# Performance work log

Measured on AMD Instinct MI355X. Metric: run time of the kernel, lower is better.

Reference implementation:

```python
import jax, jax.numpy as jnp
import numpy as np
import math

B, S, D, H, P = 4, 2048, 512, 8, 64
HD = D // H


def setup_inputs() -> dict:
    key = jax.random.key(0)
    ks = jax.random.split(key, 12)
    inp = {
        "query": jax.random.normal(ks[0], (B, S, D), jnp.float32),
        "key": jax.random.normal(ks[1], (B, S, D), jnp.float32),
        "value": jax.random.normal(ks[2], (B, S, D), jnp.float32),
        "query_pos_em": jax.random.normal(ks[3], (B, S, P), jnp.float32),
        "key_pos_em": jax.random.normal(ks[4], (B, S, P), jnp.float32),
        "mask": jax.random.randint(ks[5], (B, S), 0, 2, jnp.int32),
        # learned params (bias=False linears, LayerNorm affine)
        "Wq": jax.random.normal(ks[6], (D, D), jnp.float32) / math.sqrt(D),
        "Wk": jax.random.normal(ks[7], (D, D), jnp.float32) / math.sqrt(D),
        "Wv": jax.random.normal(ks[8], (D, D), jnp.float32) / math.sqrt(D),
        "Wo": jax.random.normal(ks[9], (D, D), jnp.float32) / math.sqrt(D),
        "ln_gamma": jnp.ones((D,), jnp.float32),
        "ln_beta": jnp.zeros((D,), jnp.float32),
    }
    return inp


def _split_heads(x):
    # (B,S,D) -> (B,H,S,HD)
    return x.reshape(B, S, H, HD).transpose(0, 2, 1, 3)


def reference(query, key, value, query_pos_em, key_pos_em, mask,
              Wq, Wk, Wv, Wo, ln_gamma, ln_beta):
    residual = query
    q = _split_heads(query @ Wq)
    k = _split_heads(key @ Wk)
    v = _split_heads(value @ Wv)

    # positional similarity: softmax over (B,S,S)
    simi = jax.nn.softmax(jnp.einsum('bqp,bkp->bqk', query_pos_em, key_pos_em), axis=-1)

    # scaled dot-product modulated elementwise by similarity (broadcast over heads)
    prod = jnp.einsum('bhqd,bhkd->bhqk', q, k) / math.sqrt(HD)
    prod = prod * simi[:, None, :, :]

    # additive mask: (mask-1)*1e8, broadcast [:, None, None, :]
    m = (mask.astype(prod.dtype) - 1.0) * 1e8
    prod = prod + m[:, None, None, :]

    attn = jax.nn.softmax(prod, axis=-1)
    out = jnp.einsum('bhqk,bhkd->bhqd', attn, v)  # (B,H,S,HD)
    out = out.transpose(0, 2, 1, 3).reshape(B, S, D)
    out = out @ Wo  # dropout is identity in eval mode

    x = residual + out
    mu = jnp.mean(x, axis=-1, keepdims=True)
    var = jnp.var(x, axis=-1, keepdims=True)
    return (x - mu) / jnp.sqrt(var + 1e-5) * ln_gamma + ln_beta
```

## Files before the change

kernel.cpp:

```cpp
#include <hip/hip_runtime.h>
#include <hip/hip_bf16.h>

#define Bq 4
#define Sq 2048
#define Dq 512
#define Hq 8
#define HDq 64
#define Pq 64

typedef __attribute__((ext_vector_type(8))) short short8;
typedef __attribute__((ext_vector_type(4))) float f32x4;

__device__ inline unsigned short f2bf(float f) {
  unsigned int u = __float_as_uint(f);
  unsigned int r = u + 0x7FFFu + ((u >> 16) & 1u);
  return (unsigned short)(r >> 16);
}
__device__ inline float bf2f(unsigned short s) {
  return __uint_as_float(((unsigned int)s) << 16);
}
__device__ inline short8 ld8f(const float* __restrict__ p) {
  const float4 a = *(const float4*)p;
  const float4 b = *(const float4*)(p + 4);
  short8 r;
  r[0] = (short)f2bf(a.x); r[1] = (short)f2bf(a.y); r[2] = (short)f2bf(a.z); r[3] = (short)f2bf(a.w);
  r[4] = (short)f2bf(b.x); r[5] = (short)f2bf(b.y); r[6] = (short)f2bf(b.z); r[7] = (short)f2bf(b.w);
  return r;
}

__global__ __launch_bounds__(256) void prep(const float* __restrict__ qpe,
                                            const float* __restrict__ kpe,
                                            const int* __restrict__ mask,
                                            unsigned short* __restrict__ qpeb,
                                            unsigned short* __restrict__ kpeb,
                                            float* __restrict__ mb) {
  const int bid = blockIdx.x;
  if (bid < 256) {
    int i = bid * 256 + threadIdx.x;
    *(short8*)&qpeb[(size_t)i * 8] = ld8f(qpe + (size_t)i * 8);
  } else if (bid < 512) {
    int i = (bid - 256) * 256 + threadIdx.x;
    *(short8*)&kpeb[(size_t)i * 8] = ld8f(kpe + (size_t)i * 8);
  } else {
    int i = (bid - 512) * 256 + threadIdx.x;
    mb[i] = ((float)mask[i] - 1.0f) * 1.442695041e8f;
  }
}

__global__ __launch_bounds__(256) void convW4(const float* __restrict__ Wq,
                                              const float* __restrict__ Wk,
                                              const float* __restrict__ Wv,
                                              const float* __restrict__ Wo,
                                              unsigned short* __restrict__ Wqt,
                                              unsigned short* __restrict__ Wkt,
                                              unsigned short* __restrict__ Wvt,
                                              unsigned short* __restrict__ Wot) {
  __shared__ float tile[32][33];
  const int z = blockIdx.z;
  const float* W = z == 0 ? Wq : z == 1 ? Wk : z == 2 ? Wv : Wo;
  unsigned short* Wt = z == 0 ? Wqt : z == 1 ? Wkt : z == 2 ? Wvt : Wot;
  const float scale = (z == 0) ? 0.125f : 1.0f;
  const int tx = threadIdx.x & 31, ty = threadIdx.x >> 5;
  const int n0 = blockIdx.x * 32, k0 = blockIdx.y * 32;
  for (int j = 0; j < 4; ++j)
    tile[ty + j * 8][tx] = W[(size_t)(k0 + ty + j * 8) * Dq + n0 + tx];
  __syncthreads();
  for (int j = 0; j < 4; ++j)
    Wt[(size_t)(n0 + ty + j * 8) * Dq + k0 + tx] = f2bf(tile[tx][ty + j * 8] * scale);
}

__global__ __launch_bounds__(256) void gemm_qkv(const float* __restrict__ Aq,
                                                const float* __restrict__ Ak,
                                                const float* __restrict__ Av,
                                                const unsigned short* __restrict__ Wqt,
                                                const unsigned short* __restrict__ Wkt,
                                                const unsigned short* __restrict__ Wvt,
                                                unsigned short* __restrict__ Qb,
                                                unsigned short* __restrict__ Kb,
                                                unsigned short* __restrict__ VbT) {
  __shared__ unsigned short Alds[128][72];
  __shared__ unsigned short Blds[128][72];
  const int z = blockIdx.z;
  const float* Ap = z == 0 ? Aq : z == 1 ? Ak : Av;
  const unsigned short* Wt = z == 0 ? Wqt : z == 1 ? Wkt : Wvt;
  unsigned short* Cb = z == 0 ? Qb : z == 1 ? Kb : VbT;
  const bool wt = (z == 2);
  const int tid = threadIdx.x;
  const int lane = tid & 63, wv = tid >> 6;
  const int wr = wv >> 1, wc = wv & 1;
  const int l15 = lane & 15, lg = lane >> 4;
  const int row0 = blockIdx.x * 128, col0 = blockIdx.y * 128;
  f32x4 acc[4][4] = {};
  for (int k0 = 0; k0 < Dq; k0 += 64) {
    __syncthreads();
#pragma unroll
    for (int j = 0; j < 4; ++j) {
      int s = tid + j * 256;
      int r = s >> 3, c8 = (s & 7) * 8;
      const float* ap = Ap + (size_t)(row0 + r) * Dq + k0 + c8;
      float4 f0 = *(const float4*)ap;
      float4 f1 = *(const float4*)(ap + 4);
      short8 u;
      u[0] = (short)f2bf(f0.x); u[1] = (short)f2bf(f0.y);
      u[2] = (short)f2bf(f0.z); u[3] = (short)f2bf(f0.w);
      u[4] = (short)f2bf(f1.x); u[5] = (short)f2bf(f1.y);
      u[6] = (short)f2bf(f1.z); u[7] = (short)f2bf(f1.w);
      *(short8*)&Alds[r][c8] = u;
      *(uint4*)&Blds[r][c8] = *(const uint4*)&Wt[(size_t)(col0 + r) * Dq + k0 + c8];
    }
    __syncthreads();
#pragma unroll
    for (int kc = 0; kc < 2; ++kc) {
      short8 a[4], b[4];
#pragma unroll
      for (int mi = 0; mi < 4; ++mi)
        a[mi] = *(const short8*)&Alds[wr * 64 + mi * 16 + l15][kc * 32 + lg * 8];
#pragma unroll
      for (int ni = 0; ni < 4; ++ni)
        b[ni] = *(const short8*)&Blds[wc * 64 + ni * 16 + l15][kc * 32 + lg * 8];
#pragma unroll
      for (int mi = 0; mi < 4; ++mi)
#pragma unroll
        for (int ni = 0; ni < 4; ++ni)
          acc[mi][ni] = __builtin_amdgcn_mfma_f32_16x16x32_bf16(a[mi], b[ni], acc[mi][ni], 0, 0, 0);
    }
  }
  const int orow = row0 + wr * 64 + lg * 4;
  const int ocol = col0 + wc * 64 + l15;
  if (wt) {
    const int bidx = orow >> 11;
#pragma unroll
    for (int mi = 0; mi < 4; ++mi)
#pragma unroll
      for (int ni = 0; ni < 4; ++ni) {
        int gc = ocol + ni * 16;
        int s = (orow + mi * 16) & (Sq - 1);
        ushort4 w = {f2bf(acc[mi][ni][0]), f2bf(acc[mi][ni][1]),
                     f2bf(acc[mi][ni][2]), f2bf(acc[mi][ni][3])};
        *(ushort4*)&Cb[((size_t)(bidx * Dq + gc)) * Sq + s] = w;
      }
  } else {
#pragma unroll
    for (int mi = 0; mi < 4; ++mi)
#pragma unroll
      for (int ni = 0; ni < 4; ++ni)
#pragma unroll
        for (int rr = 0; rr < 4; ++rr) {
          int gr = orow + mi * 16 + rr, gc = ocol + ni * 16;
          Cb[(size_t)gr * Dq + gc] = f2bf(acc[mi][ni][rr]);
        }
  }
}

__global__ __launch_bounds__(256) void gemm_wo(const unsigned short* __restrict__ Ab,
                                               const unsigned short* __restrict__ Wt,
                                               const float* __restrict__ res,
                                               float* __restrict__ Cf) {
  __shared__ unsigned short Alds[128][72];
  __shared__ unsigned short Blds[128][72];
  const int tid = threadIdx.x;
  const int lane = tid & 63, wv = tid >> 6;
  const int wr = wv >> 1, wc = wv & 1;
  const int l15 = lane & 15, lg = lane >> 4;
  const int row0 = blockIdx.x * 128, col0 = blockIdx.y * 128;
  f32x4 acc[4][4] = {};
  for (int k0 = 0; k0 < Dq; k0 += 64) {
    __syncthreads();
#pragma unroll
    for (int j = 0; j < 4; ++j) {
      int s = tid + j * 256;
      int r = s >> 3, c8 = (s & 7) * 8;
      *(uint4*)&Alds[r][c8] = *(const uint4*)&Ab[(size_t)(row0 + r) * Dq + k0 + c8];
      *(uint4*)&Blds[r][c8] = *(const uint4*)&Wt[(size_t)(col0 + r) * Dq + k0 + c8];
    }
    __syncthreads();
#pragma unroll
    for (int kc = 0; kc < 2; ++kc) {
      short8 a[4], b[4];
#pragma unroll
      for (int mi = 0; mi < 4; ++mi)
        a[mi] = *(const short8*)&Alds[wr * 64 + mi * 16 + l15][kc * 32 + lg * 8];
#pragma unroll
      for (int ni = 0; ni < 4; ++ni)
        b[ni] = *(const short8*)&Blds[wc * 64 + ni * 16 + l15][kc * 32 + lg * 8];
#pragma unroll
      for (int mi = 0; mi < 4; ++mi)
#pragma unroll
        for (int ni = 0; ni < 4; ++ni)
          acc[mi][ni] = __builtin_amdgcn_mfma_f32_16x16x32_bf16(a[mi], b[ni], acc[mi][ni], 0, 0, 0);
    }
  }
  const int orow = row0 + wr * 64 + lg * 4;
  const int ocol = col0 + wc * 64 + l15;
#pragma unroll
  for (int mi = 0; mi < 4; ++mi)
#pragma unroll
    for (int ni = 0; ni < 4; ++ni)
#pragma unroll
      for (int rr = 0; rr < 4; ++rr) {
        int gr = orow + mi * 16 + rr, gc = ocol + ni * 16;
        Cf[(size_t)gr * Dq + gc] = acc[mi][ni][rr] + res[(size_t)gr * Dq + gc];
      }
}

__global__ __launch_bounds__(256) void possim(const unsigned short* __restrict__ qpe,
                                              const unsigned short* __restrict__ kpe,
                                              unsigned short* __restrict__ simiB,
                                              float* __restrict__ invsum) {
  __shared__ float wsum[4][16];
  const int tid = threadIdx.x, lane = tid & 63, wv = tid >> 6;
  const int l15 = lane & 15, lg = lane >> 4;
  const int b = blockIdx.y, q0 = blockIdx.x * 16;
  const unsigned short* qrow = qpe + ((size_t)(b * Sq + q0 + l15)) * Pq + lg * 8;
  short8 aq0 = *(const short8*)qrow;
  short8 aq1 = *(const short8*)(qrow + 32);
  unsigned short* sB = simiB + ((size_t)(b * (Sq / 16) + blockIdx.x)) * Sq * 16;
  float lsum[4] = {0.f, 0.f, 0.f, 0.f};
  for (int t = wv; t < Sq / 64; t += 4) {
    int k0 = t * 64;
    f32x4 sc[4] = {};
#pragma unroll
    for (int ng = 0; ng < 4; ++ng) {
      const unsigned short* krow = kpe + ((size_t)(b * Sq + k0 + ng * 16 + l15)) * Pq + lg * 8;
      short8 bk0 = *(const short8*)krow;
      short8 bk1 = *(const short8*)(krow + 32);
      sc[ng] = __builtin_amdgcn_mfma_f32_16x16x32_bf16(aq0, bk0, sc[ng], 0, 0, 0);
      sc[ng] = __builtin_amdgcn_mfma_f32_16x16x32_bf16(aq1, bk1, sc[ng], 0, 0, 0);
    }
#pragma unroll
    for (int ng = 0; ng < 4; ++ng) {
      float e0 = __expf(sc[ng][0]);
      float e1 = __expf(sc[ng][1]);
      float e2 = __expf(sc[ng][2]);
      float e3 = __expf(sc[ng][3]);
      lsum[0] += e0; lsum[1] += e1; lsum[2] += e2; lsum[3] += e3;
      ushort4 st = {f2bf(e0), f2bf(e1), f2bf(e2), f2bf(e3)};
      *(ushort4*)&sB[(size_t)(k0 + ng * 16 + l15) * 16 + lg * 4] = st;
    }
  }
  for (int rr = 0; rr < 4; ++rr)
    for (int m = 1; m < 16; m <<= 1) lsum[rr] += __shfl_xor(lsum[rr], m, 64);
  if (l15 == 0)
    for (int rr = 0; rr < 4; ++rr) wsum[wv][lg * 4 + rr] = lsum[rr];
  __syncthreads();
  if (tid < 16) {
    float tot = wsum[0][tid] + wsum[1][tid] + wsum[2][tid] + wsum[3][tid];
    invsum[b * Sq + q0 + tid] = 1.0f / tot;
  }
}

__global__ __launch_bounds__(512) void attn(const unsigned short* __restrict__ Qb,
                                            const unsigned short* __restrict__ Kb,
                                            const unsigned short* __restrict__ VbT,
                                            const unsigned short* __restrict__ simiB,
                                            const float* __restrict__ invsum,
                                            const float* __restrict__ mbias,
                                            unsigned short* __restrict__ O) {
  __shared__ unsigned short Klds[2][64][72];
  __shared__ unsigned short Vlds[2][64][72];
  __shared__ unsigned short Plds[8][16][72];
  const int tid = threadIdx.x, lane = tid & 63, wv = tid >> 6;
  const int l15 = lane & 15, lg = lane >> 4;
  const int q0 = blockIdx.x * 128, h = blockIdx.y, b = blockIdx.z;
  const int qw = q0 + wv * 16;
  const int sr = tid >> 3, sc8 = (tid & 7) * 8;
  const unsigned short* Kg = Kb + ((size_t)(b * Sq + sr)) * Dq + h * HDq + sc8;
  const unsigned short* Vg = VbT + ((size_t)(b * Dq + h * HDq + sr)) * Sq + sc8;

  const unsigned short* qp = Qb + ((size_t)(b * Sq + qw + l15)) * Dq + h * HDq + lg * 8;
  short8 aq0 = *(const short8*)qp;
  short8 aq1 = *(const short8*)(qp + 32);
  float inv2[4];
#pragma unroll
  for (int rr = 0; rr < 4; ++rr)
    inv2[rr] = invsum[b * Sq + qw + lg * 4 + rr] * 1.442695041f;
  const unsigned short* sB =
      simiB + ((size_t)(b * (Sq / 16) + blockIdx.x * 8 + wv)) * Sq * 16 + lg * 4;
  const float* Mb = mbias + b * Sq;
  const int wxor = (lg >> 1) << 3;
  const int lgs = lg ^ (l15 >> 3);

  {
    *(uint4*)&Klds[0][sr][sc8] = *(const uint4*)Kg;
    *(uint4*)&Vlds[0][sr][sc8] = *(const uint4*)Vg;
  }
  f32x4 oacc[4] = {};
  float lsum[4] = {0.f, 0.f, 0.f, 0.f};
  int cur = 0;
  for (int t = 0; t < Sq / 64; ++t) {
    const int k0 = t * 64;
    __syncthreads();
    uint4 nk0, nv0;
    const bool more = (t < Sq / 64 - 1);
    if (more) {
      nk0 = *(const uint4*)(Kg + (size_t)(k0 + 64) * Dq);
      nv0 = *(const uint4*)(Vg + (k0 + 64));
    }
    ushort4 sv4[4];
    float mbf[4];
#pragma unroll
    for (int ng = 0; ng < 4; ++ng) {
      int kk = k0 + ng * 16 + l15;
      sv4[ng] = *(const ushort4*)&sB[(size_t)kk * 16];
      mbf[ng] = Mb[kk];
    }
    f32x4 sc[4] = {};
    __builtin_amdgcn_s_setprio(1);
#pragma unroll
    for (int ng = 0; ng < 4; ++ng) {
      short8 bk0 = *(const short8*)&Klds[cur][ng * 16 + l15][lg * 8];
      short8 bk1 = *(const short8*)&Klds[cur][ng * 16 + l15][32 + lg * 8];
      sc[ng] = __builtin_amdgcn_mfma_f32_16x16x32_bf16(aq0, bk0, sc[ng], 0, 0, 0);
      sc[ng] = __builtin_amdgcn_mfma_f32_16x16x32_bf16(aq1, bk1, sc[ng], 0, 0, 0);
    }
    __builtin_amdgcn_s_setprio(0);
#pragma unroll
    for (int ng = 0; ng < 4; ++ng) {
#pragma unroll
      for (int rr = 0; rr < 4; ++rr) {
        float sv = bf2f(rr == 0 ? sv4[ng].x : rr == 1 ? sv4[ng].y : rr == 2 ? sv4[ng].z
                                                                            : sv4[ng].w);
        float p = __builtin_amdgcn_exp2f(fmaf(sc[ng][rr] * sv, inv2[rr], mbf[ng]));
        lsum[rr] += p;
        Plds[wv][lg * 4 + rr][ng * 16 + (l15 ^ wxor)] = f2bf(p);
      }
    }
    short8 pa0 = *(const short8*)&Plds[wv][l15][lgs * 8];
    short8 pa1 = *(const short8*)&Plds[wv][l15][32 + lgs * 8];
    __builtin_amdgcn_s_setprio(1);
#pragma unroll
    for (int dg = 0; dg < 4; ++dg) {
      short8 bv0 = *(const short8*)&Vlds[cur][dg * 16 + l15][lg * 8];
      short8 bv1 = *(const short8*)&Vlds[cur][dg * 16 + l15][32 + lg * 8];
      oacc[dg] = __builtin_amdgcn_mfma_f32_16x16x32_bf16(pa0, bv0, oacc[dg], 0, 0, 0);
      oacc[dg] = __builtin_amdgcn_mfma_f32_16x16x32_bf16(pa1, bv1, oacc[dg], 0, 0, 0);
    }
    __builtin_amdgcn_s_setprio(0);
    if (more) {
      *(uint4*)&Klds[cur ^ 1][sr][sc8] = nk0;
      *(uint4*)&Vlds[cur ^ 1][sr][sc8] = nv0;
      cur ^= 1;
    }
  }
#pragma unroll
  for (int rr = 0; rr < 4; ++rr)
    for (int m = 1; m < 16; m <<= 1) lsum[rr] += __shfl_xor(lsum[rr], m, 64);
#pragma unroll
  for (int dg = 0; dg < 4; ++dg)
    for (int rr = 0; rr < 4; ++rr) {
      int qg = qw + lg * 4 + rr;
      O[((size_t)(b * Sq + qg)) * Dq + h * HDq + dg * 16 + l15] = f2bf(oacc[dg][rr] / lsum[rr]);
    }
}

__global__ __launch_bounds__(256) void lnorm(float* __restrict__ X,
                                             const float* __restrict__ gamma,
                                             const float* __restrict__ beta) {
  const int tid = threadIdx.x, lane = tid & 63, wv = tid >> 6;
  const int row = blockIdx.x * 4 + wv;
  float* xr = X + (size_t)row * Dq + lane * 8;
  float4 x0 = *(float4*)xr;
  float4 x1 = *(float4*)(xr + 4);
  float s = x0.x + x0.y + x0.z + x0.w + x1.x + x1.y + x1.z + x1.w;
  float s2 = x0.x * x0.x + x0.y * x0.y + x0.z * x0.z + x0.w * x0.w +
             x1.x * x1.x + x1.y * x1.y + x1.z * x1.z + x1.w * x1.w;
  for (int m = 1; m < 64; m <<= 1) {
    s += __shfl_xor(s, m, 64);
    s2 += __shfl_xor(s2, m, 64);
  }
  float mu = s * (1.0f / 512.0f);
  float var = s2 * (1.0f / 512.0f) - mu * mu;
  float rstd = rsqrtf(var + 1e-5f);
  const float* g = gamma + lane * 8;
  const float* be = beta + lane * 8;
  float4 y0, y1;
  y0.x = (x0.x - mu) * rstd * g[0] + be[0];
  y0.y = (x0.y - mu) * rstd * g[1] + be[1];
  y0.z = (x0.z - mu) * rstd * g[2] + be[2];
  y0.w = (x0.w - mu) * rstd * g[3] + be[3];
  y1.x = (x1.x - mu) * rstd * g[4] + be[4];
  y1.y = (x1.y - mu) * rstd * g[5] + be[5];
  y1.z = (x1.z - mu) * rstd * g[6] + be[6];
  y1.w = (x1.w - mu) * rstd * g[7] + be[7];
  *(float4*)xr = y0;
  *(float4*)(xr + 4) = y1;
}

extern "C" void kernel_launch(void* const* d_in, const int* in_sizes, int n_in,
                              void* d_out, int out_size, void* d_ws, size_t ws_size,
                              hipStream_t stream) {
  const float* query = (const float*)d_in[0];
  const float* key = (const float*)d_in[1];
  const float* value = (const float*)d_in[2];
  const float* qpe = (const float*)d_in[3];
  const float* kpe = (const float*)d_in[4];
  const int* mask = (const int*)d_in[5];
  const float* Wq = (const float*)d_in[6];
  const float* Wk = (const float*)d_in[7];
  const float* Wv = (const float*)d_in[8];
  const float* Wo = (const float*)d_in[9];
  const float* gamma = (const float*)d_in[10];
  const float* beta = (const float*)d_in[11];
  float* out = (float*)d_out;

  char* ws = (char*)d_ws;
  size_t off = 0;
  unsigned short* Qb = (unsigned short*)(ws + off); off += (size_t)Bq * Sq * Dq * 2;
  unsigned short* Kb = (unsigned short*)(ws + off); off += (size_t)Bq * Sq * Dq * 2;
  unsigned short* VbT = (unsigned short*)(ws + off); off += (size_t)Bq * Sq * Dq * 2;
  unsigned short* Wqt = (unsigned short*)(ws + off); off += (size_t)Dq * Dq * 2;
  unsigned short* Wkt = (unsigned short*)(ws + off); off += (size_t)Dq * Dq * 2;
  unsigned short* Wvt = (unsigned short*)(ws + off); off += (size_t)Dq * Dq * 2;
  unsigned short* Wot = (unsigned short*)(ws + off); off += (size_t)Dq * Dq * 2;
  unsigned short* simiB = (unsigned short*)(ws + off); off += (size_t)Bq * Sq * Sq * 2;
  float* invsum = (float*)(ws + off); off += (size_t)Bq * Sq * 4;
  float* mbias = (float*)(ws + off); off += (size_t)Bq * Sq * 4;
  unsigned short* Ob = (unsigned short*)(ws + off); off += (size_t)Bq * Sq * Dq * 2;
  unsigned short* qpeb = (unsigned short*)(ws + off); off += (size_t)Bq * Sq * Pq * 2;
  unsigned short* kpeb = (unsigned short*)(ws + off); off += (size_t)Bq * Sq * Pq * 2;

  dim3 blk(256);
  prep<<<dim3(544), blk, 0, stream>>>(qpe, kpe, mask, qpeb, kpeb, mbias);
  convW4<<<dim3(16, 16, 4), blk, 0, stream>>>(Wq, Wk, Wv, Wo, Wqt, Wkt, Wvt, Wot);
  possim<<<dim3(Sq / 16, Bq), blk, 0, stream>>>(qpeb, kpeb, simiB, invsum);
  gemm_qkv<<<dim3(64, 4, 3), blk, 0, stream>>>(query, key, value, Wqt, Wkt, Wvt, Qb, Kb, VbT);
  attn<<<dim3(Sq / 128, Hq, Bq), dim3(512), 0, stream>>>(Qb, Kb, VbT, simiB, invsum, mbias, Ob);
  gemm_wo<<<dim3(64, 4), blk, 0, stream>>>(Ob, Wot, query, out);
  lnorm<<<dim3(Bq * Sq / 4), blk, 0, stream>>>(out, gamma, beta);
}
```

Baseline: 149.1 us.

## Merge independent prep and GEMM launches, register-prefetch GEMM tiles and attention inputs

Folds the prep and weight-conversion kernels into one launch, and the positional-similarity and QKV GEMM kernels into another heterogeneous launch, cutting launches from seven to five so independent work can share the GPU. The QKV and Wo GEMMs now prefetch the next K-slab from global memory into registers while the current slab is computed. The attention kernel prefetches the next tile's similarity and mask values one iteration ahead. It also drops the XOR swizzle on the P tile in LDS, which may bring back LDS bank conflicts, and the extra prefetch registers raise register pressure.

```diff
diff --git a/kernel.cpp b/kernel.cpp
--- a/kernel.cpp
+++ b/kernel.cpp
@@ -28,12 +28,21 @@
   return r;
 }
 
-__global__ __launch_bounds__(256) void prep(const float* __restrict__ qpe,
-                                            const float* __restrict__ kpe,
-                                            const int* __restrict__ mask,
-                                            unsigned short* __restrict__ qpeb,
-                                            unsigned short* __restrict__ kpeb,
-                                            float* __restrict__ mb) {
+__global__ __launch_bounds__(256) void prep_conv(const float* __restrict__ qpe,
+                                                 const float* __restrict__ kpe,
+                                                 const int* __restrict__ mask,
+                                                 const float* __restrict__ Wq,
+                                                 const float* __restrict__ Wk,
+                                                 const float* __restrict__ Wv,
+                                                 const float* __restrict__ Wo,
+                                                 unsigned short* __restrict__ qpeb,
+                                                 unsigned short* __restrict__ kpeb,
+                                                 float* __restrict__ mb,
+                                                 unsigned short* __restrict__ Wqt,
+                                                 unsigned short* __restrict__ Wkt,
+                                                 unsigned short* __restrict__ Wvt,
+                                                 unsigned short* __restrict__ Wot) {
+  __shared__ float tile[32][33];
   const int bid = blockIdx.x;
   if (bid < 256) {
     int i = bid * 256 + threadIdx.x;
@@ -41,114 +50,173 @@
   } else if (bid < 512) {
     int i = (bid - 256) * 256 + threadIdx.x;
     *(short8*)&kpeb[(size_t)i * 8] = ld8f(kpe + (size_t)i * 8);
-  } else {
+  } else if (bid < 544) {
     int i = (bid - 512) * 256 + threadIdx.x;
     mb[i] = ((float)mask[i] - 1.0f) * 1.442695041e8f;
-  }
-}
-
-__global__ __launch_bounds__(256) void convW4(const float* __restrict__ Wq,
-                                              const float* __restrict__ Wk,
-                                              const float* __restrict__ Wv,
-                                              const float* __restrict__ Wo,
-                                              unsigned short* __restrict__ Wqt,
-                                              unsigned short* __restrict__ Wkt,
-                                              unsigned short* __restrict__ Wvt,
-                                              unsigned short* __restrict__ Wot) {
-  __shared__ float tile[32][33];
-  const int z = blockIdx.z;
-  const float* W = z == 0 ? Wq : z == 1 ? Wk : z == 2 ? Wv : Wo;
-  unsigned short* Wt = z == 0 ? Wqt : z == 1 ? Wkt : z == 2 ? Wvt : Wot;
-  const float scale = (z == 0) ? 0.125f : 1.0f;
-  const int tx = threadIdx.x & 31, ty = threadIdx.x >> 5;
-  const int n0 = blockIdx.x * 32, k0 = blockIdx.y * 32;
-  for (int j = 0; j < 4; ++j)
-    tile[ty + j * 8][tx] = W[(size_t)(k0 + ty + j * 8) * Dq + n0 + tx];
-  __syncthreads();
-  for (int j = 0; j < 4; ++j)
-    Wt[(size_t)(n0 + ty + j * 8) * Dq + k0 + tx] = f2bf(tile[tx][ty + j * 8] * scale);
-}
-
-__global__ __launch_bounds__(256) void gemm_qkv(const float* __restrict__ Aq,
-                                                const float* __restrict__ Ak,
-                                                const float* __restrict__ Av,
-                                                const unsigned short* __restrict__ Wqt,
-                                                const unsigned short* __restrict__ Wkt,
-                                                const unsigned short* __restrict__ Wvt,
-                                                unsigned short* __restrict__ Qb,
-                                                unsigned short* __restrict__ Kb,
-                                                unsigned short* __restrict__ VbT) {
+  } else {
+    const int cid = bid - 544;
+    const int x = cid & 15, y = (cid >> 4) & 15, z = cid >> 8;
+    const float* W = z == 0 ? Wq : z == 1 ? Wk : z == 2 ? Wv : Wo;
+    unsigned short* Wt = z == 0 ? Wqt : z == 1 ? Wkt : z == 2 ? Wvt : Wot;
+    const float scale = (z == 0) ? 0.125f : 1.0f;
+    const int tx = threadIdx.x & 31, ty = threadIdx.x >> 5;
+    const int n0 = x * 32, k0 = y * 32;
+    for (int j = 0; j < 4; ++j)
+      tile[ty + j * 8][tx] = W[(size_t)(k0 + ty + j * 8) * Dq + n0 + tx];
+    __syncthreads();
+    for (int j = 0; j < 4; ++j)
+      Wt[(size_t)(n0 + ty + j * 8) * Dq + k0 + tx] = f2bf(tile[tx][ty + j * 8] * scale);
+  }
+}
+
+__global__ __launch_bounds__(256) void sim_qkv(const float* __restrict__ Aq,
+                                               const float* __restrict__ Ak,
+                                               const float* __restrict__ Av,
+                                               const unsigned short* __restrict__ Wqt,
+                                               const unsigned short* __restrict__ Wkt,
+                                               const unsigned short* __restrict__ Wvt,
+                                               unsigned short* __restrict__ Qb,
+                                               unsigned short* __restrict__ Kb,
+                                               unsigned short* __restrict__ VbT,
+                                               const unsigned short* __restrict__ qpe,
+                                               const unsigned short* __restrict__ kpe,
+                                               unsigned short* __restrict__ simiB,
+                                               float* __restrict__ invsum) {
   __shared__ unsigned short Alds[128][72];
   __shared__ unsigned short Blds[128][72];
-  const int z = blockIdx.z;
-  const float* Ap = z == 0 ? Aq : z == 1 ? Ak : Av;
-  const unsigned short* Wt = z == 0 ? Wqt : z == 1 ? Wkt : Wvt;
-  unsigned short* Cb = z == 0 ? Qb : z == 1 ? Kb : VbT;
-  const bool wt = (z == 2);
+  __shared__ float wsum[4][16];
+  const int bid = blockIdx.x;
   const int tid = threadIdx.x;
   const int lane = tid & 63, wv = tid >> 6;
-  const int wr = wv >> 1, wc = wv & 1;
   const int l15 = lane & 15, lg = lane >> 4;
-  const int row0 = blockIdx.x * 128, col0 = blockIdx.y * 128;
-  f32x4 acc[4][4] = {};
-  for (int k0 = 0; k0 < Dq; k0 += 64) {
-    __syncthreads();
+  if (bid < 768) {
+    const int z = bid >> 8, rem = bid & 255;
+    const int bx = rem & 63, by = rem >> 6;
+    const float* Ap = z == 0 ? Aq : z == 1 ? Ak : Av;
+    const unsigned short* Wt = z == 0 ? Wqt : z == 1 ? Wkt : Wvt;
+    unsigned short* Cb = z == 0 ? Qb : z == 1 ? Kb : VbT;
+    const bool wt = (z == 2);
+    const int wr = wv >> 1, wc = wv & 1;
+    const int row0 = bx * 128, col0 = by * 128;
+    f32x4 acc[4][4] = {};
+    float4 fA0[4], fA1[4];
+    uint4 fB[4];
 #pragma unroll
     for (int j = 0; j < 4; ++j) {
       int s = tid + j * 256;
       int r = s >> 3, c8 = (s & 7) * 8;
-      const float* ap = Ap + (size_t)(row0 + r) * Dq + k0 + c8;
-      float4 f0 = *(const float4*)ap;
-      float4 f1 = *(const float4*)(ap + 4);
-      short8 u;
-      u[0] = (short)f2bf(f0.x); u[1] = (short)f2bf(f0.y);
-      u[2] = (short)f2bf(f0.z); u[3] = (short)f2bf(f0.w);
-      u[4] = (short)f2bf(f1.x); u[5] = (short)f2bf(f1.y);
-      u[6] = (short)f2bf(f1.z); u[7] = (short)f2bf(f1.w);
-      *(short8*)&Alds[r][c8] = u;
-      *(uint4*)&Blds[r][c8] = *(const uint4*)&Wt[(size_t)(col0 + r) * Dq + k0 + c8];
-    }
+      const float* ap = Ap + (size_t)(row0 + r) * Dq + c8;
+      fA0[j] = *(const float4*)ap;
+      fA1[j] = *(const float4*)(ap + 4);
+      fB[j] = *(const uint4*)&Wt[(size_t)(col0 + r) * Dq + c8];
+    }
+    for (int k0 = 0; k0 < Dq; k0 += 64) {
+      __syncthreads();
+#pragma unroll
+      for (int j = 0; j < 4; ++j) {
+        int s = tid + j * 256;
+        int r = s >> 3, c8 = (s & 7) * 8;
+        short8 u;
+        u[0] = (short)f2bf(fA0[j].x); u[1] = (short)f2bf(fA0[j].y);
+        u[2] = (short)f2bf(fA0[j].z); u[3] = (short)f2bf(fA0[j].w);
+        u[4] = (short)f2bf(fA1[j].x); u[5] = (short)f2bf(fA1[j].y);
+        u[6] = (short)f2bf(fA1[j].z); u[7] = (short)f2bf(fA1[j].w);
+        *(short8*)&Alds[r][c8] = u;
+        *(uint4*)&Blds[r][c8] = fB[j];
+      }
+      __syncthreads();
+      if (k0 + 64 < Dq) {
+#pragma unroll
+        for (int j = 0; j < 4; ++j) {
+          int s = tid + j * 256;
+          int r = s >> 3, c8 = (s & 7) * 8;
+          const float* ap = Ap + (size_t)(row0 + r) * Dq + k0 + 64 + c8;
+          fA0[j] = *(const float4*)ap;
+          fA1[j] = *(const float4*)(ap + 4);
+          fB[j] = *(const uint4*)&Wt[(size_t)(col0 + r) * Dq + k0 + 64 + c8];
+        }
+      }
+#pragma unroll
+      for (int kc = 0; kc < 2; ++kc) {
+        short8 a[4], b[4];
+#pragma unroll
+        for (int mi = 0; mi < 4; ++mi)
+          a[mi] = *(const short8*)&Alds[wr * 64 + mi * 16 + l15][kc * 32 + lg * 8];
+#pragma unroll
+        for (int ni = 0; ni < 4; ++ni)
+          b[ni] = *(const short8*)&Blds[wc * 64 + ni * 16 + l15][kc * 32 + lg * 8];
+#pragma unroll
+        for (int mi = 0; mi < 4; ++mi)
+#pragma unroll
+          for (int ni = 0; ni < 4; ++ni)
+            acc[mi][ni] = __builtin_amdgcn_mfma_f32_16x16x32_bf16(a[mi], b[ni], acc[mi][ni], 0, 0, 0);
+      }
+    }
+    const int orow = row0 + wr * 64 + lg * 4;
+    const int ocol = col0 + wc * 64 + l15;
+    if (wt) {
+      const int bidx = orow >> 11;
+#pragma unroll
+      for (int mi = 0; mi < 4; ++mi)
+#pragma unroll
+        for (int ni = 0; ni < 4; ++ni) {
+          int gc = ocol + ni * 16;
+          int s = (orow + mi * 16) & (Sq - 1);
+          ushort4 w = {f2bf(acc[mi][ni][0]), f2bf(acc[mi][ni][1]),
+                       f2bf(acc[mi][ni][2]), f2bf(acc[mi][ni][3])};
+          *(ushort4*)&Cb[((size_t)(bidx * Dq + gc)) * Sq + s] = w;
+        }
+    } else {
+#pragma unroll
+      for (int mi = 0; mi < 4; ++mi)
+#pragma unroll
+        for (int ni = 0; ni < 4; ++ni)
+#pragma unroll
+          for (int rr = 0; rr < 4; ++rr) {
+            int gr = orow + mi * 16 + rr, gc = ocol + ni * 16;
+            Cb[(size_t)gr * Dq + gc] = f2bf(acc[mi][ni][rr]);
+          }
+    }
+  } else {
+    const int pbid = bid - 768;
+    const int qblk = pbid & 127, b = pbid >> 7;
+    const int q0 = qblk * 16;
+    const unsigned short* qrow = qpe + ((size_t)(b * Sq + q0 + l15)) * Pq + lg * 8;
+    short8 aq0 = *(const short8*)qrow;
+    short8 aq1 = *(const short8*)(qrow + 32);
+    unsigned short* sB = simiB + ((size_t)(b * (Sq / 16) + qblk)) * Sq * 16;
+    float lsum[4] = {0.f, 0.f, 0.f, 0.f};
+    for (int t = wv; t < Sq / 64; t += 4) {
+      int k0 = t * 64;
+      f32x4 sc[4] = {};
+#pragma unroll
+      for (int ng = 0; ng < 4; ++ng) {
+        const unsigned short* krow = kpe + ((size_t)(b * Sq + k0 + ng * 16 + l15)) * Pq + lg * 8;
+        short8 bk0 = *(const short8*)krow;
+        short8 bk1 = *(const short8*)(krow + 32);
+        sc[ng] = __builtin_amdgcn_mfma_f32_16x16x32_bf16(aq0, bk0, sc[ng], 0, 0, 0);
+        sc[ng] = __builtin_amdgcn_mfma_f32_16x16x32_bf16(aq1, bk1, sc[ng], 0, 0, 0);
+      }
+#pragma unroll
+      for (int ng = 0; ng < 4; ++ng) {
+        float e0 = __expf(sc[ng][0]);
+        float e1 = __expf(sc[ng][1]);
+        float e2 = __expf(sc[ng][2]);
+        float e3 = __expf(sc[ng][3]);
+        lsum[0] += e0; lsum[1] += e1; lsum[2] += e2; lsum[3] += e3;
+        ushort4 st = {f2bf(e0), f2bf(e1), f2bf(e2), f2bf(e3)};
+        *(ushort4*)&sB[(size_t)(k0 + ng * 16 + l15) * 16 + lg * 4] = st;
+      }
+    }
+    for (int rr = 0; rr < 4; ++rr)
+      for (int m = 1; m < 16; m <<= 1) lsum[rr] += __shfl_xor(lsum[rr], m, 64);
+    if (l15 == 0)
+      for (int rr = 0; rr < 4; ++rr) wsum[wv][lg * 4 + rr] = lsum[rr];
     __syncthreads();
-#pragma unroll
-    for (int kc = 0; kc < 2; ++kc) {
-      short8 a[4], b[4];
-#pragma unroll
-      for (int mi = 0; mi < 4; ++mi)
-        a[mi] = *(const short8*)&Alds[wr * 64 + mi * 16 + l15][kc * 32 + lg * 8];
-#pragma unroll
-      for (int ni = 0; ni < 4; ++ni)
-        b[ni] = *(const short8*)&Blds[wc * 64 + ni * 16 + l15][kc * 32 + lg * 8];
-#pragma unroll
-      for (int mi = 0; mi < 4; ++mi)
-#pragma unroll
-        for (int ni = 0; ni < 4; ++ni)
-          acc[mi][ni] = __builtin_amdgcn_mfma_f32_16x16x32_bf16(a[mi], b[ni], acc[mi][ni], 0, 0, 0);
-    }
-  }
-  const int orow = row0 + wr * 64 + lg * 4;
-  const int ocol = col0 + wc * 64 + l15;
-  if (wt) {
-    const int bidx = orow >> 11;
-#pragma unroll
-    for (int mi = 0; mi < 4; ++mi)
-#pragma unroll
-      for (int ni = 0; ni < 4; ++ni) {
-        int gc = ocol + ni * 16;
-        int s = (orow + mi * 16) & (Sq - 1);
-        ushort4 w = {f2bf(acc[mi][ni][0]), f2bf(acc[mi][ni][1]),
-                     f2bf(acc[mi][ni][2]), f2bf(acc[mi][ni][3])};
-        *(ushort4*)&Cb[((size_t)(bidx * Dq + gc)) * Sq + s] = w;
-      }
-  } else {
-#pragma unroll
-    for (int mi = 0; mi < 4; ++mi)
-#pragma unroll
-      for (int ni = 0; ni < 4; ++ni)
-#pragma unroll
-        for (int rr = 0; rr < 4; ++rr) {
-          int gr = orow + mi * 16 + rr, gc = ocol + ni * 16;
-          Cb[(size_t)gr * Dq + gc] = f2bf(acc[mi][ni][rr]);
-        }
+    if (tid < 16) {
+      float tot = wsum[0][tid] + wsum[1][tid] + wsum[2][tid] + wsum[3][tid];
+      invsum[b * Sq + q0 + tid] = 1.0f / tot;
+    }
   }
 }
 
@@ -164,16 +232,33 @@
   const int l15 = lane & 15, lg = lane >> 4;
   const int row0 = blockIdx.x * 128, col0 = blockIdx.y * 128;
   f32x4 acc[4][4] = {};
+  uint4 fA[4], fB[4];
+#pragma unroll
+  for (int j = 0; j < 4; ++j) {
+    int s = tid + j * 256;
+    int r = s >> 3, c8 = (s & 7) * 8;
+    fA[j] = *(const uint4*)&Ab[(size_t)(row0 + r) * Dq + c8];
+    fB[j] = *(const uint4*)&Wt[(size_t)(col0 + r) * Dq + c8];
+  }
   for (int k0 = 0; k0 < Dq; k0 += 64) {
     __syncthreads();
 #pragma unroll
     for (int j = 0; j < 4; ++j) {
       int s = tid + j * 256;
       int r = s >> 3, c8 = (s & 7) * 8;
-      *(uint4*)&Alds[r][c8] = *(const uint4*)&Ab[(size_t)(row0 + r) * Dq + k0 + c8];
-      *(uint4*)&Blds[r][c8] = *(const uint4*)&Wt[(size_t)(col0 + r) * Dq + k0 + c8];
+      *(uint4*)&Alds[r][c8] = fA[j];
+      *(uint4*)&Blds[r][c8] = fB[j];
     }
     __syncthreads();
+    if (k0 + 64 < Dq) {
+#pragma unroll
+      for (int j = 0; j < 4; ++j) {
+        int s = tid + j * 256;
+        int r = s >> 3, c8 = (s & 7) * 8;
+        fA[j] = *(const uint4*)&Ab[(size_t)(row0 + r) * Dq + k0 + 64 + c8];
+        fB[j] = *(const uint4*)&Wt[(size_t)(col0 + r) * Dq + k0 + 64 + c8];
+      }
+    }
 #pragma unroll
     for (int kc = 0; kc < 2; ++kc) {
       short8 a[4], b[4];
@@ -201,52 +286,6 @@
         int gr = orow + mi * 16 + rr, gc = ocol + ni * 16;
         Cf[(size_t)gr * Dq + gc] = acc[mi][ni][rr] + res[(size_t)gr * Dq + gc];
       }
-}
-
-__global__ __launch_bounds__(256) void possim(const unsigned short* __restrict__ qpe,
-                                              const unsigned short* __restrict__ kpe,
-                                              unsigned short* __restrict__ simiB,
-                                              float* __restrict__ invsum) {
-  __shared__ float wsum[4][16];
-  const int tid = threadIdx.x, lane = tid & 63, wv = tid >> 6;
-  const int l15 = lane & 15, lg = lane >> 4;
-  const int b = blockIdx.y, q0 = blockIdx.x * 16;
-  const unsigned short* qrow = qpe + ((size_t)(b * Sq + q0 + l15)) * Pq + lg * 8;
-  short8 aq0 = *(const short8*)qrow;
-  short8 aq1 = *(const short8*)(qrow + 32);
-  unsigned short* sB = simiB + ((size_t)(b * (Sq / 16) + blockIdx.x)) * Sq * 16;
-  float lsum[4] = {0.f, 0.f, 0.f, 0.f};
-  for (int t = wv; t < Sq / 64; t += 4) {
-    int k0 = t * 64;
-    f32x4 sc[4] = {};
-#pragma unroll
-    for (int ng = 0; ng < 4; ++ng) {
-      const unsigned short* krow = kpe + ((size_t)(b * Sq + k0 + ng * 16 + l15)) * Pq + lg * 8;
-      short8 bk0 = *(const short8*)krow;
-      short8 bk1 = *(const short8*)(krow + 32);
-      sc[ng] = __builtin_amdgcn_mfma_f32_16x16x32_bf16(aq0, bk0, sc[ng], 0, 0, 0);
-      sc[ng] = __builtin_amdgcn_mfma_f32_16x16x32_bf16(aq1, bk1, sc[ng], 0, 0, 0);
-    }
-#pragma unroll
-    for (int ng = 0; ng < 4; ++ng) {
-      float e0 = __expf(sc[ng][0]);
-      float e1 = __expf(sc[ng][1]);
-      float e2 = __expf(sc[ng][2]);
-      float e3 = __expf(sc[ng][3]);
-      lsum[0] += e0; lsum[1] += e1; lsum[2] += e2; lsum[3] += e3;
-      ushort4 st = {f2bf(e0), f2bf(e1), f2bf(e2), f2bf(e3)};
-      *(ushort4*)&sB[(size_t)(k0 + ng * 16 + l15) * 16 + lg * 4] = st;
-    }
-  }
-  for (int rr = 0; rr < 4; ++rr)
-    for (int m = 1; m < 16; m <<= 1) lsum[rr] += __shfl_xor(lsum[rr], m, 64);
-  if (l15 == 0)
-    for (int rr = 0; rr < 4; ++rr) wsum[wv][lg * 4 + rr] = lsum[rr];
-  __syncthreads();
-  if (tid < 16) {
-    float tot = wsum[0][tid] + wsum[1][tid] + wsum[2][tid] + wsum[3][tid];
-    invsum[b * Sq + q0 + tid] = 1.0f / tot;
-  }
 }
 
 __global__ __launch_bounds__(512) void attn(const unsigned short* __restrict__ Qb,
@@ -277,9 +316,15 @@
   const unsigned short* sB =
       simiB + ((size_t)(b * (Sq / 16) + blockIdx.x * 8 + wv)) * Sq * 16 + lg * 4;
   const float* Mb = mbias + b * Sq;
-  const int wxor = (lg >> 1) << 3;
-  const int lgs = lg ^ (l15 >> 3);
-
+
+  ushort4 sv4[4];
+  float mbf[4];
+#pragma unroll
+  for (int ng = 0; ng < 4; ++ng) {
+    int kk = ng * 16 + l15;
+    sv4[ng] = *(const ushort4*)&sB[(size_t)kk * 16];
+    mbf[ng] = Mb[kk];
+  }
   {
     *(uint4*)&Klds[0][sr][sc8] = *(const uint4*)Kg;
     *(uint4*)&Vlds[0][sr][sc8] = *(const uint4*)Vg;
@@ -291,18 +336,18 @@
     const int k0 = t * 64;
     __syncthreads();
     uint4 nk0, nv0;
+    ushort4 nsv[4];
+    float nmb[4];
     const bool more = (t < Sq / 64 - 1);
     if (more) {
       nk0 = *(const uint4*)(Kg + (size_t)(k0 + 64) * Dq);
       nv0 = *(const uint4*)(Vg + (k0 + 64));
-    }
-    ushort4 sv4[4];
-    float mbf[4];
-#pragma unroll
-    for (int ng = 0; ng < 4; ++ng) {
-      int kk = k0 + ng * 16 + l15;
-      sv4[ng] = *(const ushort4*)&sB[(size_t)kk * 16];
-      mbf[ng] = Mb[kk];
+#pragma unroll
+      for (int ng = 0; ng < 4; ++ng) {
+        int kk = k0 + 64 + ng * 16 + l15;
+        nsv[ng] = *(const ushort4*)&sB[(size_t)kk * 16];
+        nmb[ng] = Mb[kk];
+      }
     }
     f32x4 sc[4] = {};
     __builtin_amdgcn_s_setprio(1);
@@ -322,11 +367,11 @@
                                                                             : sv4[ng].w);
         float p = __builtin_amdgcn_exp2f(fmaf(sc[ng][rr] * sv, inv2[rr], mbf[ng]));
         lsum[rr] += p;
-        Plds[wv][lg * 4 + rr][ng * 16 + (l15 ^ wxor)] = f2bf(p);
-      }
-    }
-    short8 pa0 = *(const short8*)&Plds[wv][l15][lgs * 8];
-    short8 pa1 = *(const short8*)&Plds[wv][l15][32 + lgs * 8];
+        Plds[wv][lg * 4 + rr][ng * 16 + l15] = f2bf(p);
+      }
+    }
+    short8 pa0 = *(const short8*)&Plds[wv][l15][lg * 8];
+    short8 pa1 = *(const short8*)&Plds[wv][l15][32 + lg * 8];
     __builtin_amdgcn_s_setprio(1);
 #pragma unroll
     for (int dg = 0; dg < 4; ++dg) {
@@ -339,6 +384,11 @@
     if (more) {
       *(uint4*)&Klds[cur ^ 1][sr][sc8] = nk0;
       *(uint4*)&Vlds[cur ^ 1][sr][sc8] = nv0;
+#pragma unroll
+      for (int ng = 0; ng < 4; ++ng) {
+        sv4[ng] = nsv[ng];
+        mbf[ng] = nmb[ng];
+      }
       cur ^= 1;
     }
   }
@@ -420,10 +470,10 @@
   unsigned short* kpeb = (unsigned short*)(ws + off); off += (size_t)Bq * Sq * Pq * 2;
 
   dim3 blk(256);
-  prep<<<dim3(544), blk, 0, stream>>>(qpe, kpe, mask, qpeb, kpeb, mbias);
-  convW4<<<dim3(16, 16, 4), blk, 0, stream>>>(Wq, Wk, Wv, Wo, Wqt, Wkt, Wvt, Wot);
-  possim<<<dim3(Sq / 16, Bq), blk, 0, stream>>>(qpeb, kpeb, simiB, invsum);
-  gemm_qkv<<<dim3(64, 4, 3), blk, 0, stream>>>(query, key, value, Wqt, Wkt, Wvt, Qb, Kb, VbT);
+  prep_conv<<<dim3(544 + 1024), blk, 0, stream>>>(qpe, kpe, mask, Wq, Wk, Wv, Wo, qpeb, kpeb,
+                                                  mbias, Wqt, Wkt, Wvt, Wot);
+  sim_qkv<<<dim3(768 + 512), blk, 0, stream>>>(query, key, value, Wqt, Wkt, Wvt, Qb, Kb, VbT,
+                                               qpeb, kpeb, simiB, invsum);
   attn<<<dim3(Sq / 128, Hq, Bq), dim3(512), 0, stream>>>(Qb, Kb, VbT, simiB, invsum, mbias, Ob);
   gemm_wo<<<dim3(64, 4), blk, 0, stream>>>(Ob, Wot, query, out);
   lnorm<<<dim3(Bq * Sq / 4), blk, 0, stream>>>(out, gamma, beta);
```

New measurement: 168.1 us. +12.7%, slower.
